# Optimization experiments

Hardware: AMD Instinct MI355X
Metric: run time of the kernel (lower is better)

The kernel has to match this reference:

```python
import jax, jax.numpy as jnp
import numpy as np

WS, SS, NH = 7, 3, 16  # window_size, shift_size, num_heads


def _rel_pos_index(ws):
    coords = np.stack(np.meshgrid(np.arange(ws), np.arange(ws), indexing='ij'))  # (2, ws, ws)
    cf = coords.reshape(2, -1)                       # (2, N)
    rel = (cf[:, :, None] - cf[:, None, :]).transpose(1, 2, 0).copy()  # (N, N, 2)
    rel[:, :, 0] += ws - 1
    rel[:, :, 1] += ws - 1
    rel[:, :, 0] *= 2 * ws - 1
    return rel.sum(-1)                               # (N, N) int indices into bias table


def _attn_mask(Hp, Wp, ws, ss):
    img = np.zeros((Hp, Wp))
    slices = (slice(0, -ws), slice(-ws, -ss), slice(-ss, None))
    cnt = 0
    for h in slices:
        for w in slices:
            img[h, w] = cnt
            cnt += 1
    mw = img.reshape(Hp // ws, ws, Wp // ws, ws).transpose(0, 2, 1, 3).reshape(-1, ws * ws)  # (nW, N)
    am = mw[:, None, :] - mw[:, :, None]             # (nW, N, N)
    return np.where(am != 0, -100.0, 0.0).astype(np.float32)


def setup_inputs() -> dict:
    key = jax.random.key(0)
    k1, k2, k3, k4 = jax.random.split(key, 4)
    B, H, W, C = 16, 56, 56, 512
    return {
        'q_out': jax.random.normal(k1, (B, H, W, C), dtype=jnp.float32),
        'k_out': jax.random.normal(k2, (B, H, W, C), dtype=jnp.float32),
        'v_out': jax.random.normal(k3, (B, H, W, C), dtype=jnp.float32),
        'bias_table': 0.02 * jax.random.normal(k4, ((2 * WS - 1) ** 2, NH), dtype=jnp.float32),
        'C': C, 'H': H, 'W': W,
        'x_low_padding_h': 0, 'x_low_padding_w': 0,
    }


def reference(q_out, k_out, v_out, bias_table, C, H, W, x_low_padding_h, x_low_padding_w):
    ws, ss, nh = WS, SS, NH
    Hp, Wp = H + x_low_padding_h, W + x_low_padding_w
    B = q_out.shape[0]
    hd = C // nh
    scale = hd ** (-0.5)
    N = ws * ws

    def part(x):  # (B,Hp,Wp,C) -> (B*nW, N, C)
        x = x.reshape(B, Hp // ws, ws, Wp // ws, ws, C).transpose(0, 1, 3, 2, 4, 5)
        return x.reshape(-1, N, C)

    # cyclic shift
    sq = jnp.roll(q_out, (-ss, -ss), axis=(1, 2))
    sk = jnp.roll(k_out, (-ss, -ss), axis=(1, 2))
    sv = jnp.roll(v_out, (-ss, -ss), axis=(1, 2))

    qw, kw, vw = part(sq), part(sk), part(sv)
    B_ = qw.shape[0]
    q = qw.reshape(B_, N, nh, hd).transpose(0, 2, 1, 3) * scale  # (B_, nh, N, hd)
    k = kw.reshape(B_, N, nh, hd).transpose(0, 2, 1, 3)
    v = vw.reshape(B_, N, nh, hd).transpose(0, 2, 1, 3)

    attn = jnp.einsum('bhnd,bhmd->bhnm', q, k)  # (B_, nh, N, N)

    # relative position bias
    rpi = _rel_pos_index(ws)
    bias = bias_table[rpi.reshape(-1)].reshape(N, N, nh).transpose(2, 0, 1)  # (nh, N, N)
    attn = attn + bias[None]

    # shift mask
    am = jnp.asarray(_attn_mask(Hp, Wp, ws, ss), dtype=attn.dtype)  # (nW, N, N)
    nW = am.shape[0]
    attn = attn.reshape(B_ // nW, nW, nh, N, N) + am[None, :, None]
    attn = jax.nn.softmax(attn.reshape(B_, nh, N, N), axis=-1)

    xw = jnp.einsum('bhnm,bhmd->bhnd', attn, v).transpose(0, 2, 1, 3).reshape(B_, N, C)

    # window reverse + reverse shift
    x = xw.reshape(B, Hp // ws, Wp // ws, ws, ws, C).transpose(0, 1, 3, 2, 4, 5).reshape(B, Hp, Wp, C)
    return jnp.roll(x, (ss, ss), axis=(1, 2))
```

## Files before the change

kernel.cpp:

```cpp
#include <hip/hip_runtime.h>
#include <stdint.h>


constexpr int WSZ  = 7;
constexpr int NTOK = 49;
constexpr int NH_  = 16;
constexpr int HD_  = 32;
constexpr int SP   = 56;
constexpr int CH   = 512;
constexpr float LOG2E = 1.4426950408889634f;

typedef float  f32x4 __attribute__((ext_vector_type(4)));
typedef short  s16x8 __attribute__((ext_vector_type(8)));

union FragU { uint32_t w[4]; s16x8 v; };

__device__ inline uint32_t bf16_hibits(float x) {
    uint32_t u = __float_as_uint(x);
    u += 0x7fffu + ((u >> 16) & 1u);
    return u & 0xffff0000u;
}

__device__ inline uint32_t pk_bf16(float a, float b) {
    return (bf16_hibits(a) >> 16) | bf16_hibits(b);
}

__device__ inline void hilo_pair(float a, float b, uint32_t& wh, uint32_t& wl) {
    uint32_t ah = bf16_hibits(a), bh = bf16_hibits(b);
    wh = (ah >> 16) | bh;
    float ra = a - __uint_as_float(ah);
    float rb = b - __uint_as_float(bh);
    wl = pk_bf16(ra, rb);
}

__global__ __launch_bounds__(256)
void build_bm(const float* __restrict__ bias, float* __restrict__ bm)
{
    const int blk = blockIdx.x;
    const int h = blk >> 2, cls = blk & 3;
    for (int idx = threadIdx.x; idx < 4096; idx += 256) {
        const int q = idx >> 6, m = idx & 63;
        float val;
        if (q >= NTOK || m >= NTOK) {
            val = -1e9f;
        } else {
            const int iq = q / 7, jq = q % 7, im = m / 7, jm = m % 7;
            const int rpi = (iq - im + 6) * 13 + (jq - jm + 6);
            const float bv = bias[rpi * NH_ + h];
            const int rq = ((cls & 2) ? (iq < 4 ? 3 : 6) : 0)
                         + ((cls & 1) ? (jq < 4 ? 1 : 2) : 0);
            const int rm = ((cls & 2) ? (im < 4 ? 3 : 6) : 0)
                         + ((cls & 1) ? (jm < 4 ? 1 : 2) : 0);
            const float mask = (rq != rm) ? -100.0f : 0.0f;
            val = (bv + mask) * LOG2E - 23.0f;
        }
        bm[blk * 4096 + idx] = val;
    }
}

__global__ __launch_bounds__(256, 2)
void swin_mfma_kernel(const float* __restrict__ qg,
                      const float* __restrict__ kg,
                      const float* __restrict__ vg,
                      const float* __restrict__ bm,
                      float* __restrict__ outg)
{
    const int bid  = blockIdx.x;
    const int w    = (bid & 7) + 8 * (bid >> 5);
    const int sub  = (bid >> 3) & 3;
    const int wave = threadIdx.x >> 6;
    const int h    = sub * 4 + wave;
    const int wc   = w & 7;
    const int wr   = (w >> 3) & 7;
    const int b    = w >> 6;

    const int lane = threadIdx.x & 63;
    const int g    = lane >> 4;
    const int l16  = lane & 15;

    const int t  = lane < NTOK ? lane : NTOK - 1;
    const int it = t / 7, jt = t - 7 * it;
    int sr = wr * 7 + it + 3; if (sr >= SP) sr -= SP;
    int sc = wc * 7 + jt + 3; if (sc >= SP) sc -= SP;
    const int off_t = ((b * SP + sr) * SP + sc) * CH + h * HD_;

    int oQK[4];
#pragma unroll
    for (int tt = 0; tt < 4; ++tt)
        oQK[tt] = __shfl(off_t, 16 * tt + l16);
    int oV[16];
#pragma unroll
    for (int mc = 0; mc < 2; ++mc)
#pragma unroll
        for (int e = 0; e < 8; ++e)
            oV[8 * mc + e] = __shfl(off_t, 32 * mc + 8 * g + e);

    const int cls = ((wr == 7) ? 2 : 0) | ((wc == 7) ? 1 : 0);
    const float* bmh = bm + (h * 4 + cls) * 4096;

    float4 qa[4][2], ka[4][2];
#pragma unroll
    for (int tt = 0; tt < 4; ++tt) {
        const float* qp = qg + oQK[tt] + 8 * g;
        const float* kp = kg + oQK[tt] + 8 * g;
        qa[tt][0] = *(const float4*)qp;
        qa[tt][1] = *(const float4*)(qp + 4);
        ka[tt][0] = *(const float4*)kp;
        ka[tt][1] = *(const float4*)(kp + 4);
    }
    float va[2][2][8];
#pragma unroll
    for (int mc = 0; mc < 2; ++mc)
#pragma unroll
        for (int dh = 0; dh < 2; ++dh)
#pragma unroll
            for (int e = 0; e < 8; ++e)
                va[mc][dh][e] = vg[oV[8 * mc + e] + 16 * dh + l16];
    f32x4 bmf[4][4];
#pragma unroll
    for (int tq = 0; tq < 4; ++tq)
#pragma unroll
        for (int tk = 0; tk < 4; ++tk)
            bmf[tq][tk] = *(const f32x4*)(bmh + (16 * tq + l16) * 64 + 16 * tk + 4 * g);

    __builtin_amdgcn_sched_barrier(0);

    const float qs = 0.17677669529663687f * LOG2E;

    s16x8 Qh[4], Kh[4], Kl[4];
#pragma unroll
    for (int tt = 0; tt < 4; ++tt) {
        FragU qh, kh, kl;
        qh.w[0] = pk_bf16(qa[tt][0].x * qs, qa[tt][0].y * qs);
        qh.w[1] = pk_bf16(qa[tt][0].z * qs, qa[tt][0].w * qs);
        qh.w[2] = pk_bf16(qa[tt][1].x * qs, qa[tt][1].y * qs);
        qh.w[3] = pk_bf16(qa[tt][1].z * qs, qa[tt][1].w * qs);
        hilo_pair(ka[tt][0].x, ka[tt][0].y, kh.w[0], kl.w[0]);
        hilo_pair(ka[tt][0].z, ka[tt][0].w, kh.w[1], kl.w[1]);
        hilo_pair(ka[tt][1].x, ka[tt][1].y, kh.w[2], kl.w[2]);
        hilo_pair(ka[tt][1].z, ka[tt][1].w, kh.w[3], kl.w[3]);
        Qh[tt] = qh.v; Kh[tt] = kh.v; Kl[tt] = kl.v;
    }
    s16x8 Vb[2][2];
#pragma unroll
    for (int mc = 0; mc < 2; ++mc)
#pragma unroll
        for (int dh = 0; dh < 2; ++dh) {
            FragU fu;
#pragma unroll
            for (int wd = 0; wd < 4; ++wd)
                fu.w[wd] = pk_bf16(va[mc][dh][2 * wd], va[mc][dh][2 * wd + 1]);
            Vb[mc][dh] = fu.v;
        }

    uint32_t u0[4][4], u1[4][4];
    float inv[4];
#pragma unroll
    for (int tq = 0; tq < 4; ++tq) {
        float dsum = 0.f;
#pragma unroll
        for (int tk = 0; tk < 4; ++tk) {
            f32x4 a = bmf[tq][tk];
            a = __builtin_amdgcn_mfma_f32_16x16x32_bf16(Kl[tk], Qh[tq], a, 0, 0, 0);
            a = __builtin_amdgcn_mfma_f32_16x16x32_bf16(Kh[tk], Qh[tq], a, 0, 0, 0);
            float e0 = __builtin_amdgcn_exp2f(a[0]);
            float e1 = __builtin_amdgcn_exp2f(a[1]);
            float e2 = __builtin_amdgcn_exp2f(a[2]);
            float e3 = __builtin_amdgcn_exp2f(a[3]);
            dsum += (e0 + e1) + (e2 + e3);
            u0[tq][tk] = pk_bf16(e0, e1);
            u1[tq][tk] = pk_bf16(e2, e3);
        }
        dsum += __shfl_xor(dsum, 16);
        dsum += __shfl_xor(dsum, 32);
        inv[tq] = 1.0f / (dsum + 1e-30f);
    }

    const int srcb = 32 * (g & 1) + l16;
    const bool hiG = (lane >= 32);
    s16x8 PA[4][2];
#pragma unroll
    for (int tq = 0; tq < 4; ++tq)
#pragma unroll
        for (int mc = 0; mc < 2; ++mc) {
            FragU fu;
#pragma unroll
            for (int wd = 0; wd < 4; ++wd) {
                const int sl = srcb + 16 * (wd >> 1);
                uint32_t A, B;
                if (wd & 1) {
                    A = __shfl(u1[tq][2 * mc],     sl);
                    B = __shfl(u1[tq][2 * mc + 1], sl);
                } else {
                    A = __shfl(u0[tq][2 * mc],     sl);
                    B = __shfl(u0[tq][2 * mc + 1], sl);
                }
                fu.w[wd] = hiG ? B : A;
            }
            PA[tq][mc] = fu.v;
        }

#pragma unroll
    for (int tq = 0; tq < 4; ++tq) {
        f32x4 acc[2];
#pragma unroll
        for (int dh = 0; dh < 2; ++dh) {
            f32x4 a = {0.f, 0.f, 0.f, 0.f};
            a = __builtin_amdgcn_mfma_f32_16x16x32_bf16(PA[tq][0], Vb[0][dh], a, 0, 0, 0);
            a = __builtin_amdgcn_mfma_f32_16x16x32_bf16(PA[tq][1], Vb[1][dh], a, 0, 0, 0);
            acc[dh] = a;
        }
#pragma unroll
        for (int r = 0; r < 4; ++r) {
            const float iv = __shfl(inv[tq], 4 * g + r);
            const int oo = __shfl(off_t, 16 * tq + 4 * g + r);
            if (tq < 3 || (g == 0 && r == 0)) {
#pragma unroll
                for (int dh = 0; dh < 2; ++dh)
                    outg[oo + 16 * dh + l16] = acc[dh][r] * iv;
            }
        }
    }
}

__global__ __launch_bounds__(256)
void swin_block_scalar(const float* __restrict__ qg,
                       const float* __restrict__ kg,
                       const float* __restrict__ vg,
                       const float* __restrict__ bias,
                       float* __restrict__ outg)
{
    const int wave = __builtin_amdgcn_readfirstlane(threadIdx.x >> 6);
    const int wh   = blockIdx.x * 4 + wave;
    const int h    = wh & (NH_ - 1);
    const int w    = wh >> 4;
    const int wc   = w & 7;
    const int wr   = (w >> 3) & 7;
    const int b    = w >> 6;

    const int lane = threadIdx.x & 63;
    const int rr   = lane < NTOK ? lane : NTOK - 1;
    const int i    = rr / WSZ;
    const int j    = rr - i * WSZ;

    const int hp = wr * WSZ + i;
    const int wp = wc * WSZ + j;
    int sr = hp + 3; if (sr >= SP) sr -= SP;
    int sc = wp + 3; if (sc >= SP) sc -= SP;
    const int rowoff = ((b * SP + sr) * SP + sc) * CH + h * HD_;
    const int reg_r = (hp < 49 ? 0 : (hp < 53 ? 3 : 6))
                    + (wp < 49 ? 0 : (wp < 53 ? 1 : 2));
    const float qscale = 0.17677669529663687f * LOG2E;

    float qr[HD_];
    {
        const float4* qp = reinterpret_cast<const float4*>(qg + rowoff);
#pragma unroll
        for (int tt = 0; tt < HD_ / 4; ++tt) {
            float4 x = qp[tt];
            qr[4*tt+0] = x.x * qscale; qr[4*tt+1] = x.y * qscale;
            qr[4*tt+2] = x.z * qscale; qr[4*tt+3] = x.w * qscale;
        }
    }
    const int biaslane = (i * 13 + j) * 16 + h;
    float o[HD_];
#pragma unroll
    for (int d = 0; d < HD_; ++d) o[d] = 0.f;
    float denom = 0.f;
    const float* kb = kg + b * SP * SP * CH + h * HD_;
    const float* vb = vg + b * SP * SP * CH + h * HD_;

    for (int ic = 0; ic < WSZ; ++ic) {
        const int hpc = wr * WSZ + ic;
        int src_r = hpc + 3; if (src_r >= SP) src_r -= SP;
        const int regh_c = (hpc < 49 ? 0 : (hpc < 53 ? 3 : 6));
        const float* krow0 = kb + src_r * SP * CH;
        const float* vrow0 = vb + src_r * SP * CH;
        float e[WSZ];
#pragma unroll
        for (int u = 0; u < WSZ; ++u) {
            const int wpc = wc * WSZ + u;
            int src_c = wpc + 3; if (src_c >= SP) src_c -= SP;
            const int reg_c = regh_c + (wpc < 49 ? 0 : (wpc < 53 ? 1 : 2));
            const float* krow = krow0 + src_c * CH;
            const float bv = bias[biaslane + ((6 - ic) * 13 + (6 - u)) * 16];
            float s0 = fmaf(bv, LOG2E, (reg_r != reg_c) ? -167.26950408889634f : -23.0f);
            float s1 = 0.f, s2 = 0.f, s3 = 0.f;
#pragma unroll
            for (int d = 0; d < HD_; d += 4) {
                s0 = fmaf(qr[d+0], krow[d+0], s0);
                s1 = fmaf(qr[d+1], krow[d+1], s1);
                s2 = fmaf(qr[d+2], krow[d+2], s2);
                s3 = fmaf(qr[d+3], krow[d+3], s3);
            }
            e[u] = exp2f((s0 + s1) + (s2 + s3));
            denom += e[u];
        }
#pragma unroll
        for (int u = 0; u < WSZ; ++u) {
            const int wpc = wc * WSZ + u;
            int src_c = wpc + 3; if (src_c >= SP) src_c -= SP;
            const float* vrow = vrow0 + src_c * CH;
            const float ev = e[u];
#pragma unroll
            for (int d = 0; d < HD_; ++d) o[d] = fmaf(ev, vrow[d], o[d]);
        }
    }
    const float invd = 1.0f / denom;
    if (lane < NTOK) {
        float4* op = reinterpret_cast<float4*>(outg + rowoff);
#pragma unroll
        for (int tt = 0; tt < HD_ / 4; ++tt) {
            float4 x;
            x.x = o[4*tt+0] * invd; x.y = o[4*tt+1] * invd;
            x.z = o[4*tt+2] * invd; x.w = o[4*tt+3] * invd;
            op[tt] = x;
        }
    }
}

extern "C" void kernel_launch(void* const* d_in, const int* in_sizes, int n_in,
                              void* d_out, int out_size, void* d_ws, size_t ws_size,
                              hipStream_t stream) {
    const float* q    = (const float*)d_in[0];
    const float* k    = (const float*)d_in[1];
    const float* v    = (const float*)d_in[2];
    const float* bias = (const float*)d_in[3];
    float* out        = (float*)d_out;

    const int B   = in_sizes[0] / (SP * SP * CH);
    const int nwh = B * (SP / WSZ) * (SP / WSZ) * NH_;

    const size_t bm_bytes = (size_t)NH_ * 4 * 64 * 64 * sizeof(float);
    if (ws_size >= bm_bytes) {
        float* bm = (float*)d_ws;
        hipLaunchKernelGGL(build_bm, dim3(NH_ * 4), dim3(256), 0, stream, bias, bm);
        hipLaunchKernelGGL(swin_mfma_kernel, dim3(nwh / 4), dim3(256), 0, stream,
                           q, k, v, bm, out);
    } else {
        hipLaunchKernelGGL(swin_block_scalar, dim3(nwh / 4), dim3(256), 0, stream,
                           q, k, v, bias, out);
    }
}
```

Baseline: 113.1 us.

## Software-pipeline four window-heads per wave and drop K low-part MFMA

```diff
diff --git a/kernel.cpp b/kernel.cpp
--- a/kernel.cpp
+++ b/kernel.cpp
@@ -10,31 +10,23 @@
 constexpr int CH   = 512;
 constexpr float LOG2E = 1.4426950408889634f;
 
-typedef float  f32x4 __attribute__((ext_vector_type(4)));
-typedef short  s16x8 __attribute__((ext_vector_type(8)));
+typedef float    f32x4 __attribute__((ext_vector_type(4)));
+typedef short    s16x8 __attribute__((ext_vector_type(8)));
+typedef _Float16 f16x4 __attribute__((ext_vector_type(4)));
 
 union FragU { uint32_t w[4]; s16x8 v; };
 
-__device__ inline uint32_t bf16_hibits(float x) {
+__device__ __forceinline__ uint32_t bf16_hibits(float x) {
     uint32_t u = __float_as_uint(x);
     u += 0x7fffu + ((u >> 16) & 1u);
     return u & 0xffff0000u;
 }
-
-__device__ inline uint32_t pk_bf16(float a, float b) {
+__device__ __forceinline__ uint32_t pk_bf16(float a, float b) {
     return (bf16_hibits(a) >> 16) | bf16_hibits(b);
 }
 
-__device__ inline void hilo_pair(float a, float b, uint32_t& wh, uint32_t& wl) {
-    uint32_t ah = bf16_hibits(a), bh = bf16_hibits(b);
-    wh = (ah >> 16) | bh;
-    float ra = a - __uint_as_float(ah);
-    float rb = b - __uint_as_float(bh);
-    wl = pk_bf16(ra, rb);
-}
-
 __global__ __launch_bounds__(256)
-void build_bm(const float* __restrict__ bias, float* __restrict__ bm)
+void build_bm(const float* __restrict__ bias, _Float16* __restrict__ bm)
 {
     const int blk = blockIdx.x;
     const int h = blk >> 2, cls = blk & 3;
@@ -42,7 +34,7 @@
         const int q = idx >> 6, m = idx & 63;
         float val;
         if (q >= NTOK || m >= NTOK) {
-            val = -1e9f;
+            val = -1000.0f;
         } else {
             const int iq = q / 7, jq = q % 7, im = m / 7, jm = m % 7;
             const int rpi = (iq - im + 6) * 13 + (jq - jm + 6);
@@ -52,96 +44,78 @@
             const int rm = ((cls & 2) ? (im < 4 ? 3 : 6) : 0)
                          + ((cls & 1) ? (jm < 4 ? 1 : 2) : 0);
             const float mask = (rq != rm) ? -100.0f : 0.0f;
-            val = (bv + mask) * LOG2E - 23.0f;
-        }
-        bm[blk * 4096 + idx] = val;
-    }
-}
-
-__global__ __launch_bounds__(256, 2)
-void swin_mfma_kernel(const float* __restrict__ qg,
-                      const float* __restrict__ kg,
-                      const float* __restrict__ vg,
-                      const float* __restrict__ bm,
-                      float* __restrict__ outg)
-{
-    const int bid  = blockIdx.x;
-    const int w    = (bid & 7) + 8 * (bid >> 5);
-    const int sub  = (bid >> 3) & 3;
-    const int wave = threadIdx.x >> 6;
-    const int h    = sub * 4 + wave;
-    const int wc   = w & 7;
-    const int wr   = (w >> 3) & 7;
-    const int b    = w >> 6;
-
-    const int lane = threadIdx.x & 63;
-    const int g    = lane >> 4;
-    const int l16  = lane & 15;
-
+            val = (bv + mask) * LOG2E;
+        }
+        bm[blk * 4096 + idx] = (_Float16)val;
+    }
+}
+
+struct Raw {
+    float4 q[4][2];
+    float4 k[4][2];
+    float  v[2][2][8];
+};
+struct Frag {
+    s16x8 Qh[4], Kh[4], Vb[2][2];
+};
+
+__device__ __forceinline__ int make_off(int wh, int lane) {
+    const int h  = wh & 15;
+    const int w  = wh >> 4;
+    const int wc = w & 7, wr = (w >> 3) & 7, b = w >> 6;
     const int t  = lane < NTOK ? lane : NTOK - 1;
     const int it = t / 7, jt = t - 7 * it;
     int sr = wr * 7 + it + 3; if (sr >= SP) sr -= SP;
     int sc = wc * 7 + jt + 3; if (sc >= SP) sc -= SP;
-    const int off_t = ((b * SP + sr) * SP + sc) * CH + h * HD_;
-
+    return ((b * SP + sr) * SP + sc) * CH + h * HD_;
+}
+__device__ __forceinline__ int cls_of(int wh) {
+    const int w = wh >> 4;
+    return ((((w >> 3) & 7) == 7) ? 2 : 0) | (((w & 7) == 7) ? 1 : 0);
+}
+
+__device__ __forceinline__ void issue_qkv(const float* __restrict__ qg,
+                                          const float* __restrict__ kg,
+                                          const float* __restrict__ vg,
+                                          int off, int l16, int g, Raw& r) {
     int oQK[4];
 #pragma unroll
-    for (int tt = 0; tt < 4; ++tt)
-        oQK[tt] = __shfl(off_t, 16 * tt + l16);
+    for (int tt = 0; tt < 4; ++tt) oQK[tt] = __shfl(off, 16 * tt + l16);
     int oV[16];
 #pragma unroll
     for (int mc = 0; mc < 2; ++mc)
 #pragma unroll
-        for (int e = 0; e < 8; ++e)
-            oV[8 * mc + e] = __shfl(off_t, 32 * mc + 8 * g + e);
-
-    const int cls = ((wr == 7) ? 2 : 0) | ((wc == 7) ? 1 : 0);
-    const float* bmh = bm + (h * 4 + cls) * 4096;
-
-    float4 qa[4][2], ka[4][2];
+        for (int e = 0; e < 8; ++e) oV[8 * mc + e] = __shfl(off, 32 * mc + 8 * g + e);
 #pragma unroll
     for (int tt = 0; tt < 4; ++tt) {
         const float* qp = qg + oQK[tt] + 8 * g;
         const float* kp = kg + oQK[tt] + 8 * g;
-        qa[tt][0] = *(const float4*)qp;
-        qa[tt][1] = *(const float4*)(qp + 4);
-        ka[tt][0] = *(const float4*)kp;
-        ka[tt][1] = *(const float4*)(kp + 4);
-    }
-    float va[2][2][8];
+        r.q[tt][0] = *(const float4*)qp;  r.q[tt][1] = *(const float4*)(qp + 4);
+        r.k[tt][0] = *(const float4*)kp;  r.k[tt][1] = *(const float4*)(kp + 4);
+    }
 #pragma unroll
     for (int mc = 0; mc < 2; ++mc)
 #pragma unroll
         for (int dh = 0; dh < 2; ++dh)
 #pragma unroll
             for (int e = 0; e < 8; ++e)
-                va[mc][dh][e] = vg[oV[8 * mc + e] + 16 * dh + l16];
-    f32x4 bmf[4][4];
-#pragma unroll
-    for (int tq = 0; tq < 4; ++tq)
-#pragma unroll
-        for (int tk = 0; tk < 4; ++tk)
-            bmf[tq][tk] = *(const f32x4*)(bmh + (16 * tq + l16) * 64 + 16 * tk + 4 * g);
-
-    __builtin_amdgcn_sched_barrier(0);
-
-    const float qs = 0.17677669529663687f * LOG2E;
-
-    s16x8 Qh[4], Kh[4], Kl[4];
+                r.v[mc][dh][e] = vg[oV[8 * mc + e] + 16 * dh + l16];
+}
+
+__device__ __forceinline__ void convertQKV(const Raw& r, float qs, Frag& f) {
 #pragma unroll
     for (int tt = 0; tt < 4; ++tt) {
-        FragU qh, kh, kl;
-        qh.w[0] = pk_bf16(qa[tt][0].x * qs, qa[tt][0].y * qs);
-        qh.w[1] = pk_bf16(qa[tt][0].z * qs, qa[tt][0].w * qs);
-        qh.w[2] = pk_bf16(qa[tt][1].x * qs, qa[tt][1].y * qs);
-        qh.w[3] = pk_bf16(qa[tt][1].z * qs, qa[tt][1].w * qs);
-        hilo_pair(ka[tt][0].x, ka[tt][0].y, kh.w[0], kl.w[0]);
-        hilo_pair(ka[tt][0].z, ka[tt][0].w, kh.w[1], kl.w[1]);
-        hilo_pair(ka[tt][1].x, ka[tt][1].y, kh.w[2], kl.w[2]);
-        hilo_pair(ka[tt][1].z, ka[tt][1].w, kh.w[3], kl.w[3]);
-        Qh[tt] = qh.v; Kh[tt] = kh.v; Kl[tt] = kl.v;
-    }
-    s16x8 Vb[2][2];
+        FragU qh, kh;
+        qh.w[0] = pk_bf16(r.q[tt][0].x * qs, r.q[tt][0].y * qs);
+        qh.w[1] = pk_bf16(r.q[tt][0].z * qs, r.q[tt][0].w * qs);
+        qh.w[2] = pk_bf16(r.q[tt][1].x * qs, r.q[tt][1].y * qs);
+        qh.w[3] = pk_bf16(r.q[tt][1].z * qs, r.q[tt][1].w * qs);
+        kh.w[0] = pk_bf16(r.k[tt][0].x, r.k[tt][0].y);
+        kh.w[1] = pk_bf16(r.k[tt][0].z, r.k[tt][0].w);
+        kh.w[2] = pk_bf16(r.k[tt][1].x, r.k[tt][1].y);
+        kh.w[3] = pk_bf16(r.k[tt][1].z, r.k[tt][1].w);
+        f.Qh[tt] = qh.v; f.Kh[tt] = kh.v;
+    }
 #pragma unroll
     for (int mc = 0; mc < 2; ++mc)
 #pragma unroll
@@ -149,10 +123,23 @@
             FragU fu;
 #pragma unroll
             for (int wd = 0; wd < 4; ++wd)
-                fu.w[wd] = pk_bf16(va[mc][dh][2 * wd], va[mc][dh][2 * wd + 1]);
-            Vb[mc][dh] = fu.v;
-        }
-
+                fu.w[wd] = pk_bf16(r.v[mc][dh][2 * wd], r.v[mc][dh][2 * wd + 1]);
+            f.Vb[mc][dh] = fu.v;
+        }
+}
+
+__device__ __forceinline__ void load_bm(const _Float16* __restrict__ bmh,
+                                        int l16, int g, f16x4 (&bmr)[4][4]) {
+#pragma unroll
+    for (int tq = 0; tq < 4; ++tq)
+#pragma unroll
+        for (int tk = 0; tk < 4; ++tk)
+            bmr[tq][tk] = *(const f16x4*)(bmh + (16 * tq + l16) * 64 + 16 * tk + 4 * g);
+}
+
+__device__ __forceinline__ void do_math(const Frag& f, const f16x4 (&bmr)[4][4],
+                                        int off, int lane, int g, int l16,
+                                        float* __restrict__ outg) {
     uint32_t u0[4][4], u1[4][4];
     float inv[4];
 #pragma unroll
@@ -160,9 +147,12 @@
         float dsum = 0.f;
 #pragma unroll
         for (int tk = 0; tk < 4; ++tk) {
-            f32x4 a = bmf[tq][tk];
-            a = __builtin_amdgcn_mfma_f32_16x16x32_bf16(Kl[tk], Qh[tq], a, 0, 0, 0);
-            a = __builtin_amdgcn_mfma_f32_16x16x32_bf16(Kh[tk], Qh[tq], a, 0, 0, 0);
+            f32x4 a;
+            a[0] = (float)bmr[tq][tk][0] - 23.f;
+            a[1] = (float)bmr[tq][tk][1] - 23.f;
+            a[2] = (float)bmr[tq][tk][2] - 23.f;
+            a[3] = (float)bmr[tq][tk][3] - 23.f;
+            a = __builtin_amdgcn_mfma_f32_16x16x32_bf16(f.Kh[tk], f.Qh[tq], a, 0, 0, 0);
             float e0 = __builtin_amdgcn_exp2f(a[0]);
             float e1 = __builtin_amdgcn_exp2f(a[1]);
             float e2 = __builtin_amdgcn_exp2f(a[2]);
@@ -206,14 +196,14 @@
 #pragma unroll
         for (int dh = 0; dh < 2; ++dh) {
             f32x4 a = {0.f, 0.f, 0.f, 0.f};
-            a = __builtin_amdgcn_mfma_f32_16x16x32_bf16(PA[tq][0], Vb[0][dh], a, 0, 0, 0);
-            a = __builtin_amdgcn_mfma_f32_16x16x32_bf16(PA[tq][1], Vb[1][dh], a, 0, 0, 0);
+            a = __builtin_amdgcn_mfma_f32_16x16x32_bf16(PA[tq][0], f.Vb[0][dh], a, 0, 0, 0);
+            a = __builtin_amdgcn_mfma_f32_16x16x32_bf16(PA[tq][1], f.Vb[1][dh], a, 0, 0, 0);
             acc[dh] = a;
         }
 #pragma unroll
         for (int r = 0; r < 4; ++r) {
             const float iv = __shfl(inv[tq], 4 * g + r);
-            const int oo = __shfl(off_t, 16 * tq + 4 * g + r);
+            const int oo = __shfl(off, 16 * tq + 4 * g + r);
             if (tq < 3 || (g == 0 && r == 0)) {
 #pragma unroll
                 for (int dh = 0; dh < 2; ++dh)
@@ -221,6 +211,61 @@
             }
         }
     }
+}
+
+__global__ __launch_bounds__(256, 2)
+void swin_pipe_kernel(const float* __restrict__ qg,
+                      const float* __restrict__ kg,
+                      const float* __restrict__ vg,
+                      const _Float16* __restrict__ bm,
+                      float* __restrict__ outg)
+{
+    const int wave = threadIdx.x >> 6;
+    const int gw   = blockIdx.x * 4 + wave;
+    const int lane = threadIdx.x & 63;
+    const int g    = lane >> 4;
+    const int l16  = lane & 15;
+    const float qs = 0.17677669529663687f * LOG2E;
+
+    const int h = gw & 15;
+    const _Float16* bmhead = bm + (size_t)h * 4 * 4096;
+
+    Raw A, B;
+    Frag f;
+    f16x4 bmr[4][4];
+
+    const int wh0 = gw;
+    const int off0 = make_off(wh0, lane);
+    issue_qkv(qg, kg, vg, off0, l16, g, A);
+
+    convertQKV(A, qs, f);
+    load_bm(bmhead + cls_of(wh0) * 4096, l16, g, bmr);
+    const int wh1 = gw + 4096;
+    const int off1 = make_off(wh1, lane);
+    issue_qkv(qg, kg, vg, off1, l16, g, B);
+    __builtin_amdgcn_sched_barrier(0);
+    do_math(f, bmr, off0, lane, g, l16, outg);
+
+    convertQKV(B, qs, f);
+    load_bm(bmhead + cls_of(wh1) * 4096, l16, g, bmr);
+    const int wh2 = gw + 8192;
+    const int off2 = make_off(wh2, lane);
+    issue_qkv(qg, kg, vg, off2, l16, g, A);
+    __builtin_amdgcn_sched_barrier(0);
+    do_math(f, bmr, off1, lane, g, l16, outg);
+
+    convertQKV(A, qs, f);
+    load_bm(bmhead + cls_of(wh2) * 4096, l16, g, bmr);
+    const int wh3 = gw + 12288;
+    const int off3 = make_off(wh3, lane);
+    issue_qkv(qg, kg, vg, off3, l16, g, B);
+    __builtin_amdgcn_sched_barrier(0);
+    do_math(f, bmr, off2, lane, g, l16, outg);
+
+    convertQKV(B, qs, f);
+    load_bm(bmhead + cls_of(wh3) * 4096, l16, g, bmr);
+    __builtin_amdgcn_sched_barrier(0);
+    do_math(f, bmr, off3, lane, g, l16, outg);
 }
 
 __global__ __launch_bounds__(256)
@@ -331,11 +376,11 @@
     const int B   = in_sizes[0] / (SP * SP * CH);
     const int nwh = B * (SP / WSZ) * (SP / WSZ) * NH_;
 
-    const size_t bm_bytes = (size_t)NH_ * 4 * 64 * 64 * sizeof(float);
+    const size_t bm_bytes = (size_t)NH_ * 4 * 4096 * sizeof(_Float16);
     if (ws_size >= bm_bytes) {
-        float* bm = (float*)d_ws;
+        _Float16* bm = (_Float16*)d_ws;
         hipLaunchKernelGGL(build_bm, dim3(NH_ * 4), dim3(256), 0, stream, bias, bm);
-        hipLaunchKernelGGL(swin_mfma_kernel, dim3(nwh / 4), dim3(256), 0, stream,
+        hipLaunchKernelGGL(swin_pipe_kernel, dim3(nwh / 16), dim3(256), 0, stream,
                            q, k, v, bm, out);
     } else {
         hipLaunchKernelGGL(swin_block_scalar, dim3(nwh / 4), dim3(256), 0, stream,
```

Measured after the change: 111.6 us. No clear change (-1.3%).
